# Kernel optimization log

Hardware: AMD Instinct MI355X
Metric: run time of the kernel (lower is better)

## Reference

```python
import jax, jax.numpy as jnp
import numpy as np

SIGMA = 1.0
DELTA = 1.0
TOPK = 10
TOPK_HALF = int(np.around(TOPK / 2))  # 5
EPS = 1e-12


def _cdist(a, b):
    # Euclidean distance matrix, grad-safe sqrt at zero (matches torch.cdist values).
    d2 = (jnp.sum(a * a, axis=1)[:, None]
          + jnp.sum(b * b, axis=1)[None, :]
          - 2.0 * (a @ b.T))
    d2 = jnp.maximum(d2, 0.0)
    pos = d2 > 0.0
    return jnp.where(pos, jnp.sqrt(jnp.where(pos, d2, 1.0)), 0.0)


def _consistency_weights(t_emb):
    # Everything here is under torch.no_grad() in the original.
    N = t_emb.shape[0]
    T_dist = _cdist(t_emb, t_emb)
    W_P = jnp.exp(-(T_dist ** 2) / SIGMA)
    _, idx = jax.lax.top_k(W_P, TOPK)                      # [N, TOPK]
    rows = jnp.arange(N)[:, None]
    W_NN = jnp.zeros_like(W_P).at[rows, idx].set(1.0)      # scatter_ ones
    V = (((W_NN + W_NN.T) / 2) == 1.0).astype(W_P.dtype)   # mutual kNN (symmetric)
    # Vectorized form of the per-row python loop:
    #   W_C_tilda[i, j] = V[i, j] * (sum_k V[i, k] * V[j, k]) / sum_k V[i, k]
    deg = jnp.sum(V, axis=1)                               # >= 1 (self is always a NN)
    overlap = V @ V.T                                      # [N, N] neighbor overlap
    W_C_tilda = V * overlap / deg[:, None]
    topk_half_index = idx[:, :TOPK_HALF]                   # [N, TOPK_HALF]
    W_C_hat = jnp.mean(W_C_tilda[topk_half_index], axis=1) # gather rows, mean -> [N, N]
    W_C = (W_C_hat + W_C_hat.T) / 2
    return (W_P + W_C) / 2


def reference(s_emb, t_emb):
    # disable_mu = 0 -> s_emb NOT normalized; t_emb always normalized.
    t_norm = t_emb / jnp.maximum(
        jnp.linalg.norm(t_emb, axis=1, keepdims=True), EPS)
    N = s_emb.shape[0]
    S_dist = _cdist(s_emb, s_emb)
    S_dist = S_dist / jnp.mean(S_dist, axis=1, keepdims=True)
    W = jax.lax.stop_gradient(_consistency_weights(t_norm))
    off_diag = 1.0 - jnp.eye(N, dtype=W.dtype)
    pos_weight = W * off_diag
    neg_weight = (1.0 - W) * off_diag
    pull = jnp.maximum(S_dist, 0.0) ** 2 * pos_weight
    push = jnp.maximum(DELTA - S_dist, 0.0) ** 2 * neg_weight
    return (jnp.sum(pull) + jnp.sum(push)) / (N * (N - 1))


def setup_inputs() -> dict:
    key = jax.random.key(0)
    k1, k2 = jax.random.split(key)
    N, D = 2048, 1024
    return {
        "s_emb": jax.random.normal(k1, (N, D), dtype=jnp.float32),
        "t_emb": jax.random.normal(k2, (N, D), dtype=jnp.float32),
    }
```

## Files before the change

kernel.cpp:

```cpp
#include <hip/hip_runtime.h>
#include <math.h>

#define N_ 2048
#define D_ 1024
#define TOPK 10
#define TOPK_HALF 5
#define NTRI 528
#define INV_NORM (1.0f / ((float)N_ * (float)(N_ - 1)))

typedef __attribute__((ext_vector_type(8))) short short8;
typedef __attribute__((ext_vector_type(16))) float floatx16;

__device__ __forceinline__ short f2bf(float f) {
  unsigned u = __float_as_uint(f);
  unsigned r = (u + 0x7fffu + ((u >> 16) & 1u)) >> 16;
  return (short)r;
}
__device__ __forceinline__ float bf2f(short b) {
  return __uint_as_float(((unsigned)(unsigned short)b) << 16);
}

__device__ __forceinline__ void gld_lds16(const short* g, short* l) {
  __builtin_amdgcn_global_load_lds(
      (const __attribute__((address_space(1))) unsigned int*)(g),
      (__attribute__((address_space(3))) unsigned int*)(l), 16, 0, 0);
}

#define BAR() asm volatile("s_barrier" ::: "memory")
#define WAIT12_BAR() asm volatile("s_waitcnt vmcnt(12)\ns_barrier" ::: "memory")
#define WAIT8_BAR() asm volatile("s_waitcnt vmcnt(8)\ns_barrier" ::: "memory")
#define WAIT4_BAR() asm volatile("s_waitcnt vmcnt(4)\ns_barrier" ::: "memory")
#define WAIT0_BAR() asm volatile("s_waitcnt vmcnt(0)\ns_barrier" ::: "memory")

__global__ __launch_bounds__(256) void prep_kernel(const float* __restrict__ t,
                                                   const float* __restrict__ s,
                                                   short* __restrict__ tb,
                                                   short* __restrict__ sb,
                                                   float* __restrict__ tt,
                                                   float* __restrict__ ss,
                                                   float* __restrict__ rowsum,
                                                   float* __restrict__ out) {
  int b = blockIdx.x, tid = threadIdx.x;
  __shared__ float red[256];
  if (b == 0) {
    for (int j = tid; j < N_; j += 256) rowsum[j] = 0.f;
    if (tid == 0) out[0] = 0.f;
  }
  if (b < N_) {
    const float4* rp = (const float4*)(t + (size_t)b * D_);
    float4 v = rp[tid];
    red[tid] = v.x * v.x + v.y * v.y + v.z * v.z + v.w * v.w;
    __syncthreads();
    for (int st = 128; st > 0; st >>= 1) { if (tid < st) red[tid] += red[tid + st]; __syncthreads(); }
    float inv = 1.f / fmaxf(sqrtf(red[0]), 1e-12f);
    __syncthreads();
    float a = v.x * inv, bb = v.y * inv, c = v.z * inv, d = v.w * inv;
    uint2 pk;
    pk.x = (unsigned)(unsigned short)f2bf(a) | ((unsigned)(unsigned short)f2bf(bb) << 16);
    pk.y = (unsigned)(unsigned short)f2bf(c) | ((unsigned)(unsigned short)f2bf(d) << 16);
    ((uint2*)(tb + (size_t)b * D_))[tid] = pk;
    red[tid] = a * a + bb * bb + c * c + d * d;
    __syncthreads();
    for (int st = 128; st > 0; st >>= 1) { if (tid < st) red[tid] += red[tid + st]; __syncthreads(); }
    if (tid == 0) tt[b] = red[0];
  } else {
    int row = b - N_;
    const float4* rp = (const float4*)(s + (size_t)row * D_);
    float4 v = rp[tid];
    uint2 pk;
    pk.x = (unsigned)(unsigned short)f2bf(v.x) | ((unsigned)(unsigned short)f2bf(v.y) << 16);
    pk.y = (unsigned)(unsigned short)f2bf(v.z) | ((unsigned)(unsigned short)f2bf(v.w) << 16);
    ((uint2*)(sb + (size_t)row * D_))[tid] = pk;
    red[tid] = v.x * v.x + v.y * v.y + v.z * v.z + v.w * v.w;
    __syncthreads();
    for (int st = 128; st > 0; st >>= 1) { if (tid < st) red[tid] += red[tid + st]; __syncthreads(); }
    if (tid == 0) ss[row] = red[0];
  }
}

__global__ __launch_bounds__(256) void gram_sym_kernel(
    const short* __restrict__ Tb, const short* __restrict__ Sb,
    const float* __restrict__ tt, const float* __restrict__ ss,
    short* __restrict__ WPb, short* __restrict__ Sob,
    float* __restrict__ rowsum) {
  int p = blockIdx.x;
  const int mode = (p >= NTRI);
  int q = p - mode * NTRI;
  int bi = (int)((sqrtf(8.f * (float)q + 1.f) - 1.f) * 0.5f);
  if (bi > 31) bi = 31;
  while ((bi + 1) * (bi + 2) / 2 <= q) bi++;
  while (bi * (bi + 1) / 2 > q) bi--;
  int bj = q - bi * (bi + 1) / 2;

  const short* A = mode ? Sb : Tb;
  const float* rn = mode ? ss : tt;
  short* outb = mode ? Sob : WPb;

  __shared__ __align__(16) short smem[4 * 8192];

  int tid = threadIdx.x;
  int w = tid >> 6, lane = tid & 63;
  int i0 = bi * 64, j0 = bj * 64;
  int wr = w >> 1, wc = w & 1;
  int l32 = lane & 31, half = lane >> 5;

  floatx16 acc = {};

  int sr8 = lane >> 3;
  int gch = ((lane & 7) ^ sr8) * 8;
  const short* Ag = A + (size_t)(i0 + w * 16 + sr8) * D_ + gch;
  const short* Bg = A + (size_t)(j0 + w * 16 + sr8) * D_ + gch;
  int lloc = (w * 16 + sr8) * 64 + (lane & 7) * 8;

#define STAGE(buf, k0)                                       \
  do {                                                       \
    short* Al = smem + (buf)*8192 + lloc;                    \
    short* Bl = smem + (buf)*8192 + 4096 + lloc;             \
    gld_lds16(Ag + (k0), Al);                                \
    gld_lds16(Ag + (k0) + (size_t)8 * D_, Al + 512);         \
    gld_lds16(Bg + (k0), Bl);                                \
    gld_lds16(Bg + (k0) + (size_t)8 * D_, Bl + 512);         \
  } while (0)

  STAGE(0, 0);
  STAGE(1, 64);
  STAGE(2, 128);
#pragma unroll
  for (int it = 0; it < 16; it++) {
    if (it) BAR();
    if (it + 3 < 16) STAGE((it + 3) & 3, (it + 3) * 64);
    if (it < 13) WAIT12_BAR();
    else if (it == 13) WAIT8_BAR();
    else if (it == 14) WAIT4_BAR();
    else WAIT0_BAR();
    const short* Ab = smem + (it & 3) * 8192;
    const short* Bb = smem + (it & 3) * 8192 + 4096;
#pragma unroll
    for (int kstep = 0; kstep < 4; kstep++) {
      int cA = (((2 * kstep + half) ^ (l32 & 7)) << 3);
      short8 af = *(const short8*)&Ab[(wr * 32 + l32) * 64 + cA];
      short8 bfr = *(const short8*)&Bb[(wc * 32 + l32) * 64 + cA];
      acc = __builtin_amdgcn_mfma_f32_32x32x16_bf16(af, bfr, acc, 0, 0, 0);
    }
  }

  float ov[16];
  int jcol = j0 + wc * 32 + l32;
  float rj = rn[jcol];
#pragma unroll
  for (int reg = 0; reg < 16; reg++) {
    int rl = (reg & 3) + 8 * (reg >> 2) + 4 * half;
    int i = i0 + wr * 32 + rl;
    float d2 = fmaxf(rn[i] + rj - 2.f * acc[reg], 0.f);
    float o = mode ? sqrtf(d2) : expf(-d2);
    if (i == jcol) o = mode ? 0.f : 1.f;
    ov[reg] = o;
    outb[(size_t)i * N_ + jcol] = f2bf(o);
  }
  if (mode) {
#pragma unroll
    for (int reg = 0; reg < 16; reg++) {
      float rs = ov[reg];
      rs += __shfl_xor(rs, 1); rs += __shfl_xor(rs, 2);
      rs += __shfl_xor(rs, 4); rs += __shfl_xor(rs, 8);
      rs += __shfl_xor(rs, 16);
      if (l32 == 0) {
        int rl = (reg & 3) + 8 * (reg >> 2) + 4 * half;
        atomicAdd(&rowsum[i0 + wr * 32 + rl], rs);
      }
    }
  }

  if (bi != bj) {
    if (mode) {
      float cs = 0.f;
#pragma unroll
      for (int reg = 0; reg < 16; reg++) cs += ov[reg];
      cs += __shfl_xor(cs, 32);
      if (half == 0) atomicAdd(&rowsum[jcol], cs);
    }
    BAR();
    float* fs = (float*)smem + w * 1088;
#pragma unroll
    for (int reg = 0; reg < 16; reg++) {
      int rl = (reg & 3) + 8 * (reg >> 2) + 4 * half;
      fs[l32 * 34 + rl] = ov[reg];
    }
#pragma unroll
    for (int itx = 0; itx < 8; itx++) {
      int sidx = itx * 64 + lane;
      int lc = sidx >> 4;
      int k2 = (sidx & 15) * 2;
      float lo = fs[lc * 34 + k2];
      float hi = fs[lc * 34 + k2 + 1];
      unsigned pk = (unsigned)(unsigned short)f2bf(lo) |
                    ((unsigned)(unsigned short)f2bf(hi) << 16);
      size_t jg = (size_t)(j0 + wc * 32 + lc);
      *(unsigned*)(outb + jg * N_ + i0 + wr * 32 + k2) = pk;
    }
  }
}

__global__ __launch_bounds__(64) void topk_loss_kernel(const short* __restrict__ WPb,
                                                       const short* __restrict__ Sb,
                                                       const float* __restrict__ rowsum,
                                                       int* __restrict__ idx,
                                                       unsigned* __restrict__ mask,
                                                       float* __restrict__ out) {
  int row = blockIdx.x, lane = threadIdx.x;
  const short8* wpr = (const short8*)(WPb + (size_t)row * N_);
  const short8* sr = (const short8*)(Sb + (size_t)row * N_);
  float rminv = (float)N_ / rowsum[row];
  float w[32];
  float local = 0.f;
#pragma unroll
  for (int c4 = 0; c4 < 4; c4++) {
    short8 wp8 = wpr[lane * 4 + c4];
    short8 s8 = sr[lane * 4 + c4];
#pragma unroll
    for (int e = 0; e < 8; e++) {
      float wv = bf2f(wp8[e]);
      w[c4 * 8 + e] = wv;
      float sv = bf2f(s8[e]) * rminv;
      float d = fmaxf(1.f - sv, 0.f);
      local += d * d + 0.5f * wv * (sv * sv - d * d);
    }
  }
#pragma unroll
  for (int off = 32; off > 0; off >>= 1) local += __shfl_down(local, off);
  if (lane == 0) {
    atomicAdd(out, (local - 0.5f) * INV_NORM);
    mask[row] = 0u;
  }
  int base = lane * 32;
  int sel[TOPK];
  for (int t = 0; t < TOPK; t++) {
    float bv = -2.f; int bi = 0;
#pragma unroll
    for (int c = 0; c < 32; c++)
      if (w[c] > bv) { bv = w[c]; bi = base + c; }
#pragma unroll
    for (int off = 32; off > 0; off >>= 1) {
      float ovv = __shfl_down(bv, off);
      int oi = __shfl_down(bi, off);
      if (ovv > bv || (ovv == bv && oi < bi)) { bv = ovv; bi = oi; }
    }
    bi = __shfl(bi, 0);
    sel[t] = bi;
    bool mine = (bi >> 5) == lane;
    int cc = bi & 31;
#pragma unroll
    for (int c = 0; c < 32; c++)
      if (mine && cc == c) w[c] = -1.f;
  }
  if (lane == 0) {
#pragma unroll
    for (int t = 0; t < TOPK; t++) idx[row * TOPK + t] = sel[t];
  }
}

__global__ __launch_bounds__(256) void mutual_kernel(const int* __restrict__ idx,
                                                     unsigned* __restrict__ mask) {
  int t = blockIdx.x * 256 + threadIdx.x;
  int i = t >> 4, k = t & 15;
  if (i >= N_ || k >= TOPK) return;
  int j = idx[i * TOPK + k];
  bool mut = false;
#pragma unroll
  for (int l = 0; l < TOPK; l++) mut |= (idx[j * TOPK + l] == i);
  if (mut) atomicOr(&mask[i], 1u << k);
}

__global__ __launch_bounds__(256) void sparse_wc_kernel(
    const int* __restrict__ idx, const unsigned* __restrict__ mask,
    const short* __restrict__ Sb, const float* __restrict__ rowsum,
    float* __restrict__ out) {
  int t = blockIdx.x * 256 + threadIdx.x;
  int i = t >> 6, r = t & 63;
  float contrib = 0.f;
  if (i < N_ && r < TOPK_HALF * TOPK) {
    int mi = r / TOPK, k = r - mi * TOPK;
    int m = idx[i * TOPK + mi];
    unsigned mm = mask[m];
    if ((mm >> k) & 1u) {
      int col = idx[m * TOPK + k];
      if (col != i) {
        int dm = __popc(mm);
        unsigned mc = mask[col];
        int jm[TOPK], jc[TOPK];
#pragma unroll
        for (int l = 0; l < TOPK; l++) jm[l] = idx[m * TOPK + l];
#pragma unroll
        for (int l = 0; l < TOPK; l++) jc[l] = idx[col * TOPK + l];
        int c = 0;
#pragma unroll
        for (int a = 0; a < TOPK; a++) {
          if ((mm >> a) & 1u) {
            int na = jm[a];
#pragma unroll
            for (int b = 0; b < TOPK; b++) c += (((mc >> b) & 1u) && (jc[b] == na));
          }
        }
        float v = (float)c / (float)dm * 0.1f;
        float s1 = bf2f(Sb[(size_t)i * N_ + col]) * ((float)N_ / rowsum[i]);
        float d1 = fmaxf(1.f - s1, 0.f);
        float s2 = bf2f(Sb[(size_t)col * N_ + i]) * ((float)N_ / rowsum[col]);
        float d2 = fmaxf(1.f - s2, 0.f);
        contrib = 0.5f * v * ((s1 * s1 - d1 * d1) + (s2 * s2 - d2 * d2));
      }
    }
  }
  __shared__ float red[256];
  red[threadIdx.x] = contrib; __syncthreads();
  for (int st = 128; st > 0; st >>= 1) {
    if (threadIdx.x < st) red[threadIdx.x] += red[threadIdx.x + st];
    __syncthreads();
  }
  if (threadIdx.x == 0) atomicAdd(out, red[0] * INV_NORM);
}

extern "C" void kernel_launch(void* const* d_in, const int* in_sizes, int n_in,
                              void* d_out, int out_size, void* d_ws, size_t ws_size,
                              hipStream_t stream) {
  const float* s_emb = (const float*)d_in[0];
  const float* t_emb = (const float*)d_in[1];
  float* out = (float*)d_out;

  const size_t NN = (size_t)N_ * N_;
  const size_t ND = (size_t)N_ * D_;
  short* t_bf = (short*)d_ws;
  short* s_bf = t_bf + ND;
  short* WPb = s_bf + ND;
  short* Sb = WPb + NN;
  float* tt = (float*)(Sb + NN);
  float* ss = tt + N_;
  float* rowsum = ss + N_;
  int* idx = (int*)(rowsum + N_);
  unsigned* mask = (unsigned*)(idx + (size_t)N_ * TOPK);

  prep_kernel<<<2 * N_, 256, 0, stream>>>(t_emb, s_emb, t_bf, s_bf, tt, ss, rowsum, out);

  gram_sym_kernel<<<2 * NTRI, 256, 0, stream>>>(t_bf, s_bf, tt, ss, WPb, Sb, rowsum);

  topk_loss_kernel<<<N_, 64, 0, stream>>>(WPb, Sb, rowsum, idx, mask, out);
  mutual_kernel<<<N_ * 16 / 256, 256, 0, stream>>>(idx, mask);
  sparse_wc_kernel<<<N_ * 64 / 256, 256, 0, stream>>>(idx, mask, Sb, rowsum, out);
}
```

Before: 158.6 us.

## Enlarge symmetric Gram tiles to 128x128 with 8 waves and double buffering

The triangular Gram kernel now computes 128x128 tiles instead of 64x64, using 512 threads (8 waves). Each wave owns a 32x64 sub-tile with two MFMA accumulators that share one A fragment. The LDS pipeline shrinks from a 4-stage ring to 2-stage double buffering. Each block reuses more operand data, which cuts global/LDS load traffic per FLOP and halves the number of tiles; the costs are shallower prefetch and only 272 blocks, which fits poorly on 256 CUs.

```diff
diff --git a/kernel.cpp b/kernel.cpp
--- a/kernel.cpp
+++ b/kernel.cpp
@@ -5,7 +5,7 @@
 #define D_ 1024
 #define TOPK 10
 #define TOPK_HALF 5
-#define NTRI 528
+#define NTRI2 136
 #define INV_NORM (1.0f / ((float)N_ * (float)(N_ - 1)))
 
 typedef __attribute__((ext_vector_type(8))) short short8;
@@ -27,8 +27,6 @@
 }
 
 #define BAR() asm volatile("s_barrier" ::: "memory")
-#define WAIT12_BAR() asm volatile("s_waitcnt vmcnt(12)\ns_barrier" ::: "memory")
-#define WAIT8_BAR() asm volatile("s_waitcnt vmcnt(8)\ns_barrier" ::: "memory")
 #define WAIT4_BAR() asm volatile("s_waitcnt vmcnt(4)\ns_barrier" ::: "memory")
 #define WAIT0_BAR() asm volatile("s_waitcnt vmcnt(0)\ns_barrier" ::: "memory")
 
@@ -78,16 +76,16 @@
   }
 }
 
-__global__ __launch_bounds__(256) void gram_sym_kernel(
+__global__ __launch_bounds__(512) void gram_sym_kernel(
     const short* __restrict__ Tb, const short* __restrict__ Sb,
     const float* __restrict__ tt, const float* __restrict__ ss,
     short* __restrict__ WPb, short* __restrict__ Sob,
     float* __restrict__ rowsum) {
   int p = blockIdx.x;
-  const int mode = (p >= NTRI);
-  int q = p - mode * NTRI;
+  const int mode = (p >= NTRI2);
+  int q = p - mode * NTRI2;
   int bi = (int)((sqrtf(8.f * (float)q + 1.f) - 1.f) * 0.5f);
-  if (bi > 31) bi = 31;
+  if (bi > 15) bi = 15;
   while ((bi + 1) * (bi + 2) / 2 <= q) bi++;
   while (bi * (bi + 1) / 2 > q) bi--;
   int bj = q - bi * (bi + 1) / 2;
@@ -96,15 +94,15 @@
   const float* rn = mode ? ss : tt;
   short* outb = mode ? Sob : WPb;
 
-  __shared__ __align__(16) short smem[4 * 8192];
+  __shared__ __align__(16) short smem[2 * 16384];
 
   int tid = threadIdx.x;
   int w = tid >> 6, lane = tid & 63;
-  int i0 = bi * 64, j0 = bj * 64;
-  int wr = w >> 1, wc = w & 1;
+  int i0 = bi * 128, j0 = bj * 128;
+  int rt = w & 3, ch = w >> 2;
   int l32 = lane & 31, half = lane >> 5;
 
-  floatx16 acc = {};
+  floatx16 acc[2] = {};
 
   int sr8 = lane >> 3;
   int gch = ((lane & 7) ^ sr8) * 8;
@@ -114,8 +112,8 @@
 
 #define STAGE(buf, k0)                                       \
   do {                                                       \
-    short* Al = smem + (buf)*8192 + lloc;                    \
-    short* Bl = smem + (buf)*8192 + 4096 + lloc;             \
+    short* Al = smem + (buf)*16384 + lloc;                   \
+    short* Bl = smem + (buf)*16384 + 8192 + lloc;            \
     gld_lds16(Ag + (k0), Al);                                \
     gld_lds16(Ag + (k0) + (size_t)8 * D_, Al + 512);         \
     gld_lds16(Bg + (k0), Bl);                                \
@@ -123,80 +121,93 @@
   } while (0)
 
   STAGE(0, 0);
-  STAGE(1, 64);
-  STAGE(2, 128);
 #pragma unroll
   for (int it = 0; it < 16; it++) {
+    int cur = it & 1;
     if (it) BAR();
-    if (it + 3 < 16) STAGE((it + 3) & 3, (it + 3) * 64);
-    if (it < 13) WAIT12_BAR();
-    else if (it == 13) WAIT8_BAR();
-    else if (it == 14) WAIT4_BAR();
-    else WAIT0_BAR();
-    const short* Ab = smem + (it & 3) * 8192;
-    const short* Bb = smem + (it & 3) * 8192 + 4096;
+    if (it < 15) {
+      STAGE(!cur, (it + 1) * 64);
+      WAIT4_BAR();
+    } else {
+      WAIT0_BAR();
+    }
+    const short* Ab = smem + cur * 16384;
+    const short* Bb = smem + cur * 16384 + 8192;
 #pragma unroll
     for (int kstep = 0; kstep < 4; kstep++) {
-      int cA = (((2 * kstep + half) ^ (l32 & 7)) << 3);
-      short8 af = *(const short8*)&Ab[(wr * 32 + l32) * 64 + cA];
-      short8 bfr = *(const short8*)&Bb[(wc * 32 + l32) * 64 + cA];
-      acc = __builtin_amdgcn_mfma_f32_32x32x16_bf16(af, bfr, acc, 0, 0, 0);
-    }
-  }
-
-  float ov[16];
-  int jcol = j0 + wc * 32 + l32;
-  float rj = rn[jcol];
-#pragma unroll
-  for (int reg = 0; reg < 16; reg++) {
-    int rl = (reg & 3) + 8 * (reg >> 2) + 4 * half;
-    int i = i0 + wr * 32 + rl;
-    float d2 = fmaxf(rn[i] + rj - 2.f * acc[reg], 0.f);
-    float o = mode ? sqrtf(d2) : expf(-d2);
-    if (i == jcol) o = mode ? 0.f : 1.f;
-    ov[reg] = o;
-    outb[(size_t)i * N_ + jcol] = f2bf(o);
+      int cb = 2 * kstep + half;
+      int phys = ((cb ^ (l32 & 7)) << 3);
+      short8 af = *(const short8*)&Ab[(rt * 32 + l32) * 64 + phys];
+      short8 b0 = *(const short8*)&Bb[(ch * 64 + l32) * 64 + phys];
+      short8 b1 = *(const short8*)&Bb[(ch * 64 + 32 + l32) * 64 + phys];
+      acc[0] = __builtin_amdgcn_mfma_f32_32x32x16_bf16(af, b0, acc[0], 0, 0, 0);
+      acc[1] = __builtin_amdgcn_mfma_f32_32x32x16_bf16(af, b1, acc[1], 0, 0, 0);
+    }
+  }
+
+  float ov[2][16];
+  int ibase = i0 + rt * 32;
+#pragma unroll
+  for (int nt = 0; nt < 2; nt++) {
+    int jcol = j0 + ch * 64 + nt * 32 + l32;
+    float rj = rn[jcol];
+#pragma unroll
+    for (int reg = 0; reg < 16; reg++) {
+      int rl = (reg & 3) + 8 * (reg >> 2) + 4 * half;
+      int i = ibase + rl;
+      float d2 = fmaxf(rn[i] + rj - 2.f * acc[nt][reg], 0.f);
+      float o = mode ? sqrtf(d2) : expf(-d2);
+      if (i == jcol) o = mode ? 0.f : 1.f;
+      ov[nt][reg] = o;
+      outb[(size_t)i * N_ + jcol] = f2bf(o);
+    }
   }
   if (mode) {
 #pragma unroll
     for (int reg = 0; reg < 16; reg++) {
-      float rs = ov[reg];
+      float rs = ov[0][reg] + ov[1][reg];
       rs += __shfl_xor(rs, 1); rs += __shfl_xor(rs, 2);
       rs += __shfl_xor(rs, 4); rs += __shfl_xor(rs, 8);
       rs += __shfl_xor(rs, 16);
       if (l32 == 0) {
         int rl = (reg & 3) + 8 * (reg >> 2) + 4 * half;
-        atomicAdd(&rowsum[i0 + wr * 32 + rl], rs);
+        atomicAdd(&rowsum[ibase + rl], rs);
       }
     }
   }
 
   if (bi != bj) {
     if (mode) {
-      float cs = 0.f;
-#pragma unroll
-      for (int reg = 0; reg < 16; reg++) cs += ov[reg];
-      cs += __shfl_xor(cs, 32);
-      if (half == 0) atomicAdd(&rowsum[jcol], cs);
+#pragma unroll
+      for (int nt = 0; nt < 2; nt++) {
+        float cs = 0.f;
+#pragma unroll
+        for (int reg = 0; reg < 16; reg++) cs += ov[nt][reg];
+        cs += __shfl_xor(cs, 32);
+        if (half == 0) atomicAdd(&rowsum[j0 + ch * 64 + nt * 32 + l32], cs);
+      }
     }
     BAR();
     float* fs = (float*)smem + w * 1088;
 #pragma unroll
-    for (int reg = 0; reg < 16; reg++) {
-      int rl = (reg & 3) + 8 * (reg >> 2) + 4 * half;
-      fs[l32 * 34 + rl] = ov[reg];
-    }
-#pragma unroll
-    for (int itx = 0; itx < 8; itx++) {
-      int sidx = itx * 64 + lane;
-      int lc = sidx >> 4;
-      int k2 = (sidx & 15) * 2;
-      float lo = fs[lc * 34 + k2];
-      float hi = fs[lc * 34 + k2 + 1];
-      unsigned pk = (unsigned)(unsigned short)f2bf(lo) |
-                    ((unsigned)(unsigned short)f2bf(hi) << 16);
-      size_t jg = (size_t)(j0 + wc * 32 + lc);
-      *(unsigned*)(outb + jg * N_ + i0 + wr * 32 + k2) = pk;
+    for (int nt = 0; nt < 2; nt++) {
+#pragma unroll
+      for (int reg = 0; reg < 16; reg++) {
+        int rl = (reg & 3) + 8 * (reg >> 2) + 4 * half;
+        fs[l32 * 34 + rl] = ov[nt][reg];
+      }
+#pragma unroll
+      for (int itx = 0; itx < 8; itx++) {
+        int sidx = itx * 64 + lane;
+        int lc = sidx >> 4;
+        int k2 = (sidx & 15) * 2;
+        float lo = fs[lc * 34 + k2];
+        float hi = fs[lc * 34 + k2 + 1];
+        unsigned pk = (unsigned)(unsigned short)f2bf(lo) |
+                      ((unsigned)(unsigned short)f2bf(hi) << 16);
+        size_t jg = (size_t)(j0 + ch * 64 + nt * 32 + lc);
+        *(unsigned*)(outb + jg * N_ + ibase + k2) = pk;
+      }
     }
   }
 }
@@ -340,7 +351,7 @@
 
   prep_kernel<<<2 * N_, 256, 0, stream>>>(t_emb, s_emb, t_bf, s_bf, tt, ss, rowsum, out);
 
-  gram_sym_kernel<<<2 * NTRI, 256, 0, stream>>>(t_bf, s_bf, tt, ss, WPb, Sb, rowsum);
+  gram_sym_kernel<<<2 * NTRI2, 512, 0, stream>>>(t_bf, s_bf, tt, ss, WPb, Sb, rowsum);
 
   topk_loss_kernel<<<N_, 64, 0, stream>>>(WPb, Sb, rowsum, idx, mask, out);
   mutual_kernel<<<N_ * 16 / 256, 256, 0, stream>>>(idx, mask);
```

Measured after the change: 150.2 us. 1.06x faster.
